# Kernel tuning notes

Measured on AMD Instinct MI355X. Metric: run time of the kernel, lower is better.

Reference implementation:

```python
import jax, jax.numpy as jnp
import numpy as np
from jax import lax

# Grid / layer constants matching init_kwargs
D, H, W = 41, 159, 159   # spatial_shape (chosen so (dim-K) % S == 0)
K = 3                    # kernel_size
S = 2                    # stride
CIN, COUT = 32, 64       # in_channels, out_channels
B = 2                    # batch_size
N_PER_BATCH = 75000      # active voxels per batch element (unique coords)


def setup_inputs() -> dict:
    # Unique active-voxel coordinates per batch (spconv assumes no duplicates).
    rng = np.random.default_rng(0)
    nvox = D * H * W
    rows = []
    for b in range(B):
        lin = rng.choice(nvox, size=N_PER_BATCH, replace=False)
        z = lin // (H * W)
        y = (lin // W) % H
        x = lin % W
        rows.append(np.stack([np.full(N_PER_BATCH, b), z, y, x], axis=1))
    coors = jnp.asarray(np.concatenate(rows, axis=0), dtype=jnp.int32)  # [N,4]

    key = jax.random.key(0)
    k1, k2, k3 = jax.random.split(key, 3)
    features = jax.random.normal(k1, (B * N_PER_BATCH, CIN), dtype=jnp.float32)
    # SparseConv3d weight (no bias): kernel [K,K,K,CIN,COUT] in DHWIO layout.
    w1 = (jax.random.normal(k2, (K, K, K, CIN, COUT), dtype=jnp.float32) * 0.05)
    # SparseInverseConv3d weight: transpose-conv mapping COUT -> CIN; stored in
    # forward-conv DHWIO layout [K,K,K,CIN,COUT] and applied via conv_transpose
    # with transpose_kernel=True (the exact adjoint of the forward conv op).
    w2 = (jax.random.normal(k3, (K, K, K, CIN, COUT), dtype=jnp.float32) * 0.05)
    return {"features": features, "coors": coors, "batch_size": B, "w1": w1, "w2": w2}


def reference(features, coors, batch_size, w1, w2):
    # Scatter active features into a dense NDHWC grid (equivalent to the sparse
    # tensor; SparseConv3d with bias=False gives identical values on active sites).
    b, z, y, x = coors[:, 0], coors[:, 1], coors[:, 2], coors[:, 3]
    dense = jnp.zeros((batch_size, D, H, W, CIN), features.dtype).at[b, z, y, x].set(features)
    # Mask of originally-active sites: SparseInverseConv3d (shared indice_key)
    # only produces outputs at these sites, and ToDense zeros everything else.
    mask = jnp.zeros((batch_size, D, H, W, 1), features.dtype).at[b, z, y, x].set(1.0)

    dn = ("NDHWC", "DHWIO", "NDHWC")
    # SparseConv3d(CIN->COUT, k=3, s=2): strided VALID conv.
    mid = lax.conv_general_dilated(dense, w1, (S, S, S), "VALID", dimension_numbers=dn)
    # SparseInverseConv3d(COUT->CIN): exact transpose of the forward conv's
    # gather/scatter pattern; recovers the original spatial shape.
    back = lax.conv_transpose(mid, w2, (S, S, S), "VALID", dimension_numbers=dn,
                              transpose_kernel=True)
    out = back * mask  # restrict to original active sites, zeros elsewhere
    return jnp.transpose(out, (0, 4, 1, 2, 3))  # ToDense returns NCDHW
```

## Files before the change

kernel.cpp:

```cpp
#include <hip/hip_runtime.h>

#define D_   41
#define H_   159
#define W_   159
#define MD   20
#define MH   79
#define MW   79
#define CIN  32
#define COUT 64
#define BATCH 2

#define NTAP 27
#define PW   17
#define WLDS (NTAP * 64 * PW)

typedef unsigned int u32;

static __device__ __forceinline__ u32 bf16_rn(float x) {
    u32 u = __float_as_uint(x);
    return (u + 0x7fffu + ((u >> 16) & 1u)) >> 16;
}
static __device__ __forceinline__ float bf_lo(u32 p) { return __uint_as_float(p << 16); }
static __device__ __forceinline__ float bf_hi(u32 p) { return __uint_as_float(p & 0xffff0000u); }

__global__ void pack_kernel(const float* __restrict__ w1, const float* __restrict__ w2,
                            u32* __restrict__ w1p, u32* __restrict__ w2p) {
    int i = blockIdx.x * 256 + threadIdx.x;
    if (i >= WLDS) return;
    int j = i % PW;
    int r = i / PW;
    int co = r & 63, t = r >> 6;
    if (j >= 16) { w1p[i] = 0; w2p[i] = 0; return; }
    int s0 = (t * 32 + 2 * j) * 64 + co;
    int s1 = (t * 32 + 2 * j + 1) * 64 + co;
    w1p[i] = bf16_rn(w1[s0]) | (bf16_rn(w1[s1]) << 16);
    w2p[i] = bf16_rn(w2[s0]) | (bf16_rn(w2[s1]) << 16);
}

__global__ void scatter_idx_kernel(const int* __restrict__ coors,
                                   int* __restrict__ idx, int n) {
    int i = blockIdx.x * blockDim.x + threadIdx.x;
    if (i >= n) return;
    int4 c = ((const int4*)coors)[i];
    idx[((c.x * D_ + c.y) * H_ + c.z) * W_ + c.w] = i;
}

__global__ __launch_bounds__(1024) void mid_kernel(const float* __restrict__ feat,
                                                   const int* __restrict__ idx,
                                                   const u32* __restrict__ w1p,
                                                   float* __restrict__ mid) {
    __shared__ u32 lw[WLDS];
    for (int i = threadIdx.x; i < WLDS; i += 1024) lw[i] = w1p[i];
    __syncthreads();

    const int NV = BATCH * MD * MH * MW;
    int lane = threadIdx.x & 63;
    int wid  = threadIdx.x >> 6;
    int nw   = gridDim.x * 16;
    int gw   = blockIdx.x * 16 + wid;
    int per  = (NV + nw - 1) / nw;
    int v0   = gw * per;
    int v1   = v0 + per; if (v1 > NV) v1 = NV;

    int l  = lane < NTAP ? lane : NTAP - 1;
    int kz = l / 9, kr = l % 9, ky = kr / 3, kx = kr % 3;

    for (int v = v0; v < v1; ++v) {
        int xo = v % MW; int t0 = v / MW;
        int yo = t0 % MH; t0 /= MH;
        int zo = t0 % MD; int b = t0 / MD;

        int p = -1;
        if (lane < NTAP)
            p = idx[((b * D_ + 2 * zo + kz) * H_ + 2 * yo + ky) * W_ + 2 * xo + kx];
        unsigned long long m = __ballot(p >= 0);

        float acc0 = 0.f, acc1 = 0.f;
        while (m) {
            int t = __builtin_ctzll(m);
            m &= m - 1;
            int pp = __shfl(p, t);
            const float4* f4 = (const float4*)(feat + (size_t)pp * CIN);
            const u32* w = lw + (t * 64 + lane) * PW;
            #pragma unroll
            for (int jq = 0; jq < 8; ++jq) {
                float4 f = f4[jq];
                u32 p0 = w[2 * jq + 0];
                u32 p1 = w[2 * jq + 1];
                acc0 = fmaf(f.x, bf_lo(p0), acc0);
                acc1 = fmaf(f.y, bf_hi(p0), acc1);
                acc0 = fmaf(f.z, bf_lo(p1), acc0);
                acc1 = fmaf(f.w, bf_hi(p1), acc1);
            }
        }
        mid[(size_t)v * COUT + lane] = acc0 + acc1;
    }
}

#define BSTEP(MK, HALF)                                            \
    {                                                              \
        bool up = (lane & MK) != 0;                                \
        _Pragma("unroll")                                          \
        for (int k = 0; k < HALF; ++k) {                           \
            float send = up ? acc[k] : acc[k + HALF];              \
            float keep = up ? acc[k + HALF] : acc[k];              \
            acc[k] = keep + __shfl_xor(send, MK, 64);              \
        }                                                          \
    }

__global__ __launch_bounds__(1024) void out_kernel(const int* __restrict__ coors,
                                                   const float* __restrict__ mid,
                                                   const u32* __restrict__ w2p,
                                                   float* __restrict__ out, int n) {
    __shared__ u32 lw[WLDS];
    for (int i = threadIdx.x; i < WLDS; i += 1024) lw[i] = w2p[i];
    __syncthreads();

    int lane = threadIdx.x & 63;
    int wid  = threadIdx.x >> 6;
    int nw   = gridDim.x * 16;
    int gw   = blockIdx.x * 16 + wid;
    int per  = (n + nw - 1) / nw;
    int i0   = gw * per;
    int i1   = i0 + per; if (i1 > n) i1 = n;

    int l  = lane < NTAP ? lane : NTAP - 1;
    int kz = l / 9, kr = l % 9, ky = kr / 3, kx = kr % 3;

    for (int i = i0; i < i1; ++i) {
        int4 c = ((const int4*)coors)[i];
        int b = c.x, z = c.y, y = c.z, x = c.w;

        int zr = z - kz, yr = y - ky, xr = x - kx;
        bool ok = (lane < NTAP) &&
                  zr >= 0 && !(zr & 1) && (zr >> 1) < MD &&
                  yr >= 0 && !(yr & 1) && (yr >> 1) < MH &&
                  xr >= 0 && !(xr & 1) && (xr >> 1) < MW;
        int vv = ok ? ((b * MD + (zr >> 1)) * MH + (yr >> 1)) * MW + (xr >> 1) : -1;
        unsigned long long m = __ballot(ok);

        float acc[CIN];
        #pragma unroll
        for (int ci = 0; ci < CIN; ++ci) acc[ci] = 0.f;

        while (m) {
            int t = __builtin_ctzll(m);
            m &= m - 1;
            int v = __shfl(vv, t);
            float mr = mid[(size_t)v * COUT + lane];
            const u32* w = lw + (t * 64 + lane) * PW;
            #pragma unroll
            for (int j = 0; j < 16; ++j) {
                u32 pw = w[j];
                acc[2 * j + 0] = fmaf(mr, bf_lo(pw), acc[2 * j + 0]);
                acc[2 * j + 1] = fmaf(mr, bf_hi(pw), acc[2 * j + 1]);
            }
        }

        BSTEP(32, 16)
        BSTEP(16, 8)
        BSTEP(8, 4)
        BSTEP(4, 2)
        BSTEP(2, 1)
        float s = acc[0] + __shfl_xor(acc[0], 1, 64);
        if (!(lane & 1)) {
            int ci = lane >> 1;
            out[((size_t)(b * CIN + ci) * D_ + z) * (H_ * W_) + (size_t)y * W_ + x] = s;
        }
    }
}

extern "C" void kernel_launch(void* const* d_in, const int* in_sizes, int n_in,
                              void* d_out, int out_size, void* d_ws, size_t ws_size,
                              hipStream_t stream) {
    const float* feat  = (const float*)d_in[0];
    const int*   coors = (const int*)d_in[1];
    const float* w1    = (const float*)d_in[3];
    const float* w2    = (const float*)d_in[4];
    float*       out   = (float*)d_out;

    int n = in_sizes[0] / CIN;

    int*   idx      = (int*)d_ws;
    size_t idxBytes = (size_t)BATCH * D_ * H_ * W_ * sizeof(int);
    size_t midOff   = (idxBytes + 255) & ~(size_t)255;
    float* mid      = (float*)((char*)d_ws + midOff);
    size_t wOff     = midOff + (size_t)BATCH * MD * MH * MW * COUT * sizeof(float);
    wOff            = (wOff + 255) & ~(size_t)255;
    u32*   w1p      = (u32*)((char*)d_ws + wOff);
    u32*   w2p      = w1p + WLDS;

    hipMemsetAsync(idx, 0xFF, idxBytes, stream);
    hipMemsetAsync(d_out, 0, (size_t)out_size * sizeof(float), stream);

    pack_kernel<<<(WLDS + 255) / 256, 256, 0, stream>>>(w1, w2, w1p, w2p);
    scatter_idx_kernel<<<(n + 255) / 256, 256, 0, stream>>>(coors, idx, n);

    mid_kernel<<<256, 1024, 0, stream>>>(feat, idx, w1p, mid);
    out_kernel<<<256, 1024, 0, stream>>>(coors, mid, w2p, out, n);
}
```

Baseline: 648.2 us.

## Pipeline gathers: pair voxels and taps, prefetch indices, transpose LDS weight layout

The packed weight layout in LDS changes from a padded per-lane row (stride 17) to a tap-major, co-contiguous layout, so each lane reads consecutive words across lanes without padding. The mid kernel processes two output voxels per iteration, prefetching the next pair's neighbour indices and issuing both gathers before the FMAs. The out kernel prefetches the next coordinate and handles two taps per loop trip, to raise memory-level parallelism and hide gather latency. In exchange, register pressure rises, which may lower occupancy at 1024-thread blocks.

```diff
diff --git a/kernel.cpp b/kernel.cpp
--- a/kernel.cpp
+++ b/kernel.cpp
@@ -11,8 +11,7 @@
 #define BATCH 2
 
 #define NTAP 27
-#define PW   17
-#define WLDS (NTAP * 64 * PW)
+#define WLDS (NTAP * 16 * 64)
 
 typedef unsigned int u32;
 
@@ -27,10 +26,7 @@
                             u32* __restrict__ w1p, u32* __restrict__ w2p) {
     int i = blockIdx.x * 256 + threadIdx.x;
     if (i >= WLDS) return;
-    int j = i % PW;
-    int r = i / PW;
-    int co = r & 63, t = r >> 6;
-    if (j >= 16) { w1p[i] = 0; w2p[i] = 0; return; }
+    int co = i & 63, j = (i >> 6) & 15, t = i >> 10;
     int s0 = (t * 32 + 2 * j) * 64 + co;
     int s1 = (t * 32 + 2 * j + 1) * 64 + co;
     w1p[i] = bf16_rn(w1[s0]) | (bf16_rn(w1[s1]) << 16);
@@ -65,35 +61,68 @@
     int l  = lane < NTAP ? lane : NTAP - 1;
     int kz = l / 9, kr = l % 9, ky = kr / 3, kx = kr % 3;
 
-    for (int v = v0; v < v1; ++v) {
+    auto probe = [&](int v) -> int {
+        if (v >= v1 || lane >= NTAP) return -1;
         int xo = v % MW; int t0 = v / MW;
         int yo = t0 % MH; t0 /= MH;
         int zo = t0 % MD; int b = t0 / MD;
-
-        int p = -1;
-        if (lane < NTAP)
-            p = idx[((b * D_ + 2 * zo + kz) * H_ + 2 * yo + ky) * W_ + 2 * xo + kx];
-        unsigned long long m = __ballot(p >= 0);
-
-        float acc0 = 0.f, acc1 = 0.f;
-        while (m) {
-            int t = __builtin_ctzll(m);
-            m &= m - 1;
-            int pp = __shfl(p, t);
-            const float4* f4 = (const float4*)(feat + (size_t)pp * CIN);
-            const u32* w = lw + (t * 64 + lane) * PW;
-            #pragma unroll
-            for (int jq = 0; jq < 8; ++jq) {
-                float4 f = f4[jq];
-                u32 p0 = w[2 * jq + 0];
-                u32 p1 = w[2 * jq + 1];
-                acc0 = fmaf(f.x, bf_lo(p0), acc0);
-                acc1 = fmaf(f.y, bf_hi(p0), acc1);
-                acc0 = fmaf(f.z, bf_lo(p1), acc0);
-                acc1 = fmaf(f.w, bf_hi(p1), acc1);
+        return idx[((b * D_ + 2 * zo + kz) * H_ + 2 * yo + ky) * W_ + 2 * xo + kx];
+    };
+
+    int pA = probe(v0), pB = probe(v0 + 1);
+    for (int v = v0; v < v1; v += 2) {
+        int cA = pA, cB = pB;
+        pA = probe(v + 2);
+        pB = probe(v + 3);
+        unsigned long long mA = __ballot(cA >= 0);
+        unsigned long long mB = __ballot(cB >= 0);
+
+        float a0 = 0.f, a1 = 0.f, b0 = 0.f, b1 = 0.f;
+        while (mA | mB) {
+            bool hA = mA != 0, hB = mB != 0;
+            float4 fav[8], fbv[8];
+            u32 wav[16], wbv[16];
+            if (hA) {
+                int t = (int)__builtin_ctzll(mA); mA &= mA - 1;
+                int pp = __shfl(cA, t);
+                const float4* f4 = (const float4*)(feat + (size_t)pp * CIN);
+                const u32* w = lw + (t * 16) * 64 + lane;
+                #pragma unroll
+                for (int q = 0; q < 8; ++q) fav[q] = f4[q];
+                #pragma unroll
+                for (int j = 0; j < 16; ++j) wav[j] = w[j * 64];
+            }
+            if (hB) {
+                int t = (int)__builtin_ctzll(mB); mB &= mB - 1;
+                int pp = __shfl(cB, t);
+                const float4* f4 = (const float4*)(feat + (size_t)pp * CIN);
+                const u32* w = lw + (t * 16) * 64 + lane;
+                #pragma unroll
+                for (int q = 0; q < 8; ++q) fbv[q] = f4[q];
+                #pragma unroll
+                for (int j = 0; j < 16; ++j) wbv[j] = w[j * 64];
+            }
+            if (hA) {
+                #pragma unroll
+                for (int q = 0; q < 8; ++q) {
+                    a0 = fmaf(fav[q].x, bf_lo(wav[2 * q + 0]), a0);
+                    a1 = fmaf(fav[q].y, bf_hi(wav[2 * q + 0]), a1);
+                    a0 = fmaf(fav[q].z, bf_lo(wav[2 * q + 1]), a0);
+                    a1 = fmaf(fav[q].w, bf_hi(wav[2 * q + 1]), a1);
+                }
+            }
+            if (hB) {
+                #pragma unroll
+                for (int q = 0; q < 8; ++q) {
+                    b0 = fmaf(fbv[q].x, bf_lo(wbv[2 * q + 0]), b0);
+                    b1 = fmaf(fbv[q].y, bf_hi(wbv[2 * q + 0]), b1);
+                    b0 = fmaf(fbv[q].z, bf_lo(wbv[2 * q + 1]), b0);
+                    b1 = fmaf(fbv[q].w, bf_hi(wbv[2 * q + 1]), b1);
+                }
             }
         }
-        mid[(size_t)v * COUT + lane] = acc0 + acc1;
+        mid[(size_t)v * COUT + lane] = a0 + a1;
+        if (v + 1 < v1) mid[(size_t)(v + 1) * COUT + lane] = b0 + b1;
     }
 }
 
@@ -127,8 +156,13 @@
     int l  = lane < NTAP ? lane : NTAP - 1;
     int kz = l / 9, kr = l % 9, ky = kr / 3, kx = kr % 3;
 
+    const int4* cvec = (const int4*)coors;
+    int4 nc = make_int4(0, 0, 0, 0);
+    if (i0 < i1) nc = cvec[i0];
+
     for (int i = i0; i < i1; ++i) {
-        int4 c = ((const int4*)coors)[i];
+        int4 c = nc;
+        if (i + 1 < i1) nc = cvec[i + 1];
         int b = c.x, z = c.y, y = c.z, x = c.w;
 
         int zr = z - kz, yr = y - ky, xr = x - kx;
@@ -144,16 +178,38 @@
         for (int ci = 0; ci < CIN; ++ci) acc[ci] = 0.f;
 
         while (m) {
-            int t = __builtin_ctzll(m);
-            m &= m - 1;
-            int v = __shfl(vv, t);
-            float mr = mid[(size_t)v * COUT + lane];
-            const u32* w = lw + (t * 64 + lane) * PW;
+            int t0 = (int)__builtin_ctzll(m); m &= m - 1;
+            bool h1 = (m != 0);
+            int t1 = 0;
+            if (h1) { t1 = (int)__builtin_ctzll(m); m &= m - 1; }
+
+            int ve0 = __shfl(vv, t0);
+            float mr0 = mid[(size_t)ve0 * COUT + lane];
+            u32 wv0[16];
+            const u32* w0 = lw + (t0 * 16) * 64 + lane;
+            #pragma unroll
+            for (int j = 0; j < 16; ++j) wv0[j] = w0[j * 64];
+
+            float mr1 = 0.f; u32 wv1[16];
+            if (h1) {
+                int ve1 = __shfl(vv, t1);
+                mr1 = mid[(size_t)ve1 * COUT + lane];
+                const u32* w1_ = lw + (t1 * 16) * 64 + lane;
+                #pragma unroll
+                for (int j = 0; j < 16; ++j) wv1[j] = w1_[j * 64];
+            }
+
             #pragma unroll
             for (int j = 0; j < 16; ++j) {
-                u32 pw = w[j];
-                acc[2 * j + 0] = fmaf(mr, bf_lo(pw), acc[2 * j + 0]);
-                acc[2 * j + 1] = fmaf(mr, bf_hi(pw), acc[2 * j + 1]);
+                acc[2 * j + 0] = fmaf(mr0, bf_lo(wv0[j]), acc[2 * j + 0]);
+                acc[2 * j + 1] = fmaf(mr0, bf_hi(wv0[j]), acc[2 * j + 1]);
+            }
+            if (h1) {
+                #pragma unroll
+                for (int j = 0; j < 16; ++j) {
+                    acc[2 * j + 0] = fmaf(mr1, bf_lo(wv1[j]), acc[2 * j + 0]);
+                    acc[2 * j + 1] = fmaf(mr1, bf_hi(wv1[j]), acc[2 * j + 1]);
+                }
             }
         }
 
```

Result: faster. 634.0 us (-2.2%).
